# Kernel tuning notes

Measured on AMD Instinct MI355X. Metric: run time of the kernel, lower is better.

## Reference

```python
import jax, jax.numpy as jnp
import numpy as np

N_EMBD = 768
N_HEAD = 12
HEAD_DIM = N_EMBD // N_HEAD
B, T = 2, 2048
EPS = 1e-5


def setup_inputs() -> dict:
    key = jax.random.key(0)
    ks = jax.random.split(key, 16)
    s = 0.02
    return {
        "x": jax.random.normal(ks[0], (B, T, N_EMBD), dtype=jnp.float32),
        "ln1_g": jnp.ones((N_EMBD,), jnp.float32),
        "ln1_b": jnp.zeros((N_EMBD,), jnp.float32),
        "W_attn": jax.random.normal(ks[1], (N_EMBD, 3 * N_EMBD), jnp.float32) * s,
        "b_attn": jnp.zeros((3 * N_EMBD,), jnp.float32),
        "W_cproj": jax.random.normal(ks[2], (N_EMBD, N_EMBD), jnp.float32) * s,
        "b_cproj": jnp.zeros((N_EMBD,), jnp.float32),
        "ln2_g": jnp.ones((N_EMBD,), jnp.float32),
        "ln2_b": jnp.zeros((N_EMBD,), jnp.float32),
        "W_fc": jax.random.normal(ks[3], (N_EMBD, 4 * N_EMBD), jnp.float32) * s,
        "b_fc": jnp.zeros((4 * N_EMBD,), jnp.float32),
        "W_mproj": jax.random.normal(ks[4], (4 * N_EMBD, N_EMBD), jnp.float32) * s,
        "b_mproj": jnp.zeros((N_EMBD,), jnp.float32),
    }


def _layernorm(x, g, b):
    mu = jnp.mean(x, axis=-1, keepdims=True)
    var = jnp.mean(jnp.square(x - mu), axis=-1, keepdims=True)
    return (x - mu) * jax.lax.rsqrt(var + EPS) * g + b


def _attention(h, W_attn, b_attn, W_cproj, b_cproj):
    Bx, Tx, C = h.shape
    qkv = h @ W_attn + b_attn  # [B, T, 3C]
    q, k, v = jnp.split(qkv, 3, axis=-1)
    # [B, H, T, D]
    def split_heads(t):
        return t.reshape(Bx, Tx, N_HEAD, HEAD_DIM).transpose(0, 2, 1, 3)
    q, k, v = split_heads(q), split_heads(k), split_heads(v)
    att = jnp.einsum("bhqd,bhkd->bhqk", q, k) / np.sqrt(HEAD_DIM).astype(np.float32)
    causal = jnp.tril(jnp.ones((Tx, Tx), dtype=bool))
    att = jnp.where(causal, att, jnp.float32(-jnp.inf))
    att = jax.nn.softmax(att, axis=-1)
    y = jnp.einsum("bhqk,bhkd->bhqd", att, v)
    y = y.transpose(0, 2, 1, 3).reshape(Bx, Tx, C)
    return y @ W_cproj + b_cproj


def _mlp(h, W_fc, b_fc, W_mproj, b_mproj):
    return jax.nn.gelu(h @ W_fc + b_fc, approximate=False) @ W_mproj + b_mproj


def reference(x, ln1_g, ln1_b, W_attn, b_attn, W_cproj, b_cproj,
              ln2_g, ln2_b, W_fc, b_fc, W_mproj, b_mproj):
    x = x + _attention(_layernorm(x, ln1_g, ln1_b), W_attn, b_attn, W_cproj, b_cproj)
    x = x + _mlp(_layernorm(x, ln2_g, ln2_b), W_fc, b_fc, W_mproj, b_mproj)
    return x
```

## Files before the change

kernel.cpp:

```cpp
#include <hip/hip_runtime.h>
#include <cstdint>
#include <cstddef>

#define B_ 2
#define T_ 2048
#define C_ 768
#define H_ 12
#define D_ 64

typedef __attribute__((ext_vector_type(8))) short s16x8;
typedef __attribute__((ext_vector_type(4))) float fx4;

static __device__ __forceinline__ unsigned short f2bf(float f) {
  unsigned u = __builtin_bit_cast(unsigned, f);
  unsigned r = u + 0x7fffu + ((u >> 16) & 1u);
  return (unsigned short)(r >> 16);
}
static __device__ __forceinline__ unsigned short f2bf_trunc(float f) {
  return (unsigned short)(__builtin_bit_cast(unsigned, f) >> 16);
}

static __device__ __forceinline__ void glds16(const unsigned short* g, unsigned short* l) {
  __builtin_amdgcn_global_load_lds(
      (const __attribute__((address_space(1))) void*)(g),
      (__attribute__((address_space(3))) void*)(l), 16, 0, 0);
}

__global__ __launch_bounds__(256) void prep(
    const float* __restrict__ Wattn, const float* __restrict__ Wcproj,
    const float* __restrict__ Wfc, const float* __restrict__ Wmproj,
    unsigned short* __restrict__ WattnT, unsigned short* __restrict__ WcprojT,
    unsigned short* __restrict__ WfcT, unsigned short* __restrict__ WmprojT,
    const float* __restrict__ X, const float* __restrict__ g,
    const float* __restrict__ bb, unsigned short* __restrict__ O) {
  __shared__ float tile[32][33];
  __shared__ float ps[8];
  int bid = blockIdx.x, tid = threadIdx.x;
  if (bid < 6912) {
    const float* W; unsigned short* Wt; int R, C, idx;
    if (bid < 1728)      { W = Wattn;  Wt = WattnT;  R = 768;  C = 2304; idx = bid; }
    else if (bid < 2304) { W = Wcproj; Wt = WcprojT; R = 768;  C = 768;  idx = bid - 1728; }
    else if (bid < 4608) { W = Wfc;    Wt = WfcT;    R = 768;  C = 3072; idx = bid - 2304; }
    else                 { W = Wmproj; Wt = WmprojT; R = 3072; C = 768;  idx = bid - 4608; }
    int ct = C >> 5;
    int c0 = (idx % ct) * 32, r0 = (idx / ct) * 32;
    int tx = tid & 31, ty = tid >> 5;
#pragma unroll
    for (int i = 0; i < 4; ++i)
      tile[ty + i * 8][tx] = W[(size_t)(r0 + ty + i * 8) * C + (c0 + tx)];
    __syncthreads();
#pragma unroll
    for (int i = 0; i < 4; ++i)
      Wt[(size_t)(c0 + ty + i * 8) * R + (r0 + tx)] = f2bf(tile[tx][ty + i * 8]);
  } else {
    int row = bid - 6912;
    const float* xr = X + (size_t)row * C_;
    float v0 = xr[tid], v1 = xr[tid + 256], v2 = xr[tid + 512];
    float s = v0 + v1 + v2;
    float s2 = v0 * v0 + v1 * v1 + v2 * v2;
#pragma unroll
    for (int off = 1; off < 64; off <<= 1) {
      s += __shfl_xor(s, off);
      s2 += __shfl_xor(s2, off);
    }
    int wv = tid >> 6;
    if ((tid & 63) == 0) { ps[wv] = s; ps[wv + 4] = s2; }
    __syncthreads();
    s = ps[0] + ps[1] + ps[2] + ps[3];
    s2 = ps[4] + ps[5] + ps[6] + ps[7];
    float mu = s * (1.f / C_);
    float var = s2 * (1.f / C_) - mu * mu;
    float rstd = rsqrtf(var + 1e-5f);
    unsigned short* orow = O + (size_t)row * C_;
    orow[tid]       = f2bf((v0 - mu) * rstd * g[tid]       + bb[tid]);
    orow[tid + 256] = f2bf((v1 - mu) * rstd * g[tid + 256] + bb[tid + 256]);
    orow[tid + 512] = f2bf((v2 - mu) * rstd * g[tid + 512] + bb[tid + 512]);
  }
}

__global__ __launch_bounds__(256) void layernorm_bf16(
    const float* __restrict__ X, const float* __restrict__ g,
    const float* __restrict__ bb, unsigned short* __restrict__ O) {
  int row = blockIdx.x, tid = threadIdx.x;
  const float* xr = X + (size_t)row * C_;
  float v0 = xr[tid], v1 = xr[tid + 256], v2 = xr[tid + 512];
  float s = v0 + v1 + v2;
  float s2 = v0 * v0 + v1 * v1 + v2 * v2;
#pragma unroll
  for (int off = 1; off < 64; off <<= 1) {
    s += __shfl_xor(s, off);
    s2 += __shfl_xor(s2, off);
  }
  __shared__ float ps[8];
  int wv = tid >> 6;
  if ((tid & 63) == 0) { ps[wv] = s; ps[wv + 4] = s2; }
  __syncthreads();
  s = ps[0] + ps[1] + ps[2] + ps[3];
  s2 = ps[4] + ps[5] + ps[6] + ps[7];
  float mu = s * (1.f / C_);
  float var = s2 * (1.f / C_) - mu * mu;
  float rstd = rsqrtf(var + 1e-5f);
  unsigned short* orow = O + (size_t)row * C_;
  orow[tid]       = f2bf((v0 - mu) * rstd * g[tid]       + bb[tid]);
  orow[tid + 256] = f2bf((v1 - mu) * rstd * g[tid + 256] + bb[tid + 256]);
  orow[tid + 512] = f2bf((v2 - mu) * rstd * g[tid + 512] + bb[tid + 512]);
}

template <int BM, int BN, int BK, int MODE>
__global__ __launch_bounds__(256) void gemm_db(
    const unsigned short* __restrict__ A, const unsigned short* __restrict__ Bt,
    const float* __restrict__ bias, const float* __restrict__ resid,
    float* __restrict__ outF, unsigned short* __restrict__ outB,
    unsigned short* __restrict__ qO, unsigned short* __restrict__ kO,
    unsigned short* __restrict__ vtO, int M, int N, int K) {
  constexpr int AT = BM / 32;
  constexpr int BT = BN / 32;
  constexpr int KS = BK / 32;
  constexpr int CA = BM * BK / 2048;
  constexpr int CB = BN * BK / 2048;
  constexpr int ASZ = BM * BK, BSZ = BN * BK;
  constexpr bool SWIZ = (BK == 64);
  __shared__ __align__(16) unsigned short As[2 * ASZ];
  __shared__ __align__(16) unsigned short Bs[2 * BSZ];
  int tid = threadIdx.x;
  int wv = tid >> 6, lane = tid & 63, quad = lane >> 4, l15 = lane & 15;
  int wm = wv >> 1, wn = wv & 1;
  int m0, n0;
  if (MODE == 1) { m0 = blockIdx.x * BM; n0 = blockIdx.y * BN; }
  else           { n0 = blockIdx.x * BN; m0 = blockIdx.y * BM; }
  fx4 acc[AT][BT];
#pragma unroll
  for (int i = 0; i < AT; ++i)
#pragma unroll
    for (int j = 0; j < BT; ++j) acc[i][j] = fx4{0.f, 0.f, 0.f, 0.f};

  int nk = K / BK;
#pragma unroll
  for (int i = 0; i < CA; ++i) {
    int e = (i * 256 + tid) * 8;
    int row = e / BK, col = e & (BK - 1);
    if (SWIZ) col = (((col >> 3) ^ (row & 7)) << 3);
    glds16(&A[(size_t)(m0 + row) * K + col], &As[(i * 256 + (tid & ~63)) * 8]);
  }
#pragma unroll
  for (int i = 0; i < CB; ++i) {
    int e = (i * 256 + tid) * 8;
    int row = e / BK, col = e & (BK - 1);
    if (SWIZ) col = (((col >> 3) ^ (row & 7)) << 3);
    glds16(&Bt[(size_t)(n0 + row) * K + col], &Bs[(i * 256 + (tid & ~63)) * 8]);
  }
  for (int kt = 0; kt < nk; ++kt) {
    int cur = kt & 1;
    __syncthreads();
    if (kt + 1 < nk) {
      int kb = (kt + 1) * BK;
      int nxt = cur ^ 1;
#pragma unroll
      for (int i = 0; i < CA; ++i) {
        int e = (i * 256 + tid) * 8;
        int row = e / BK, col = e & (BK - 1);
        if (SWIZ) col = (((col >> 3) ^ (row & 7)) << 3);
        glds16(&A[(size_t)(m0 + row) * K + kb + col],
               &As[nxt * ASZ + (i * 256 + (tid & ~63)) * 8]);
      }
#pragma unroll
      for (int i = 0; i < CB; ++i) {
        int e = (i * 256 + tid) * 8;
        int row = e / BK, col = e & (BK - 1);
        if (SWIZ) col = (((col >> 3) ^ (row & 7)) << 3);
        glds16(&Bt[(size_t)(n0 + row) * K + kb + col],
               &Bs[nxt * BSZ + (i * 256 + (tid & ~63)) * 8]);
      }
    }
#pragma unroll
    for (int ks = 0; ks < KS; ++ks) {
      s16x8 af[AT], bf[BT];
#pragma unroll
      for (int mt = 0; mt < AT; ++mt) {
        int r = wm * (BM / 2) + mt * 16 + l15;
        int c = ks * 32 + quad * 8;
        if (SWIZ) c = (((c >> 3) ^ (r & 7)) << 3);
        af[mt] = *(const s16x8*)&As[cur * ASZ + r * BK + c];
      }
#pragma unroll
      for (int nt = 0; nt < BT; ++nt) {
        int r = wn * (BN / 2) + nt * 16 + l15;
        int c = ks * 32 + quad * 8;
        if (SWIZ) c = (((c >> 3) ^ (r & 7)) << 3);
        bf[nt] = *(const s16x8*)&Bs[cur * BSZ + r * BK + c];
      }
#pragma unroll
      for (int mt = 0; mt < AT; ++mt)
#pragma unroll
        for (int nt = 0; nt < BT; ++nt)
          acc[mt][nt] = __builtin_amdgcn_mfma_f32_16x16x32_bf16(af[mt], bf[nt], acc[mt][nt], 0, 0, 0);
    }
  }

#pragma unroll
  for (int mt = 0; mt < AT; ++mt)
#pragma unroll
    for (int nt = 0; nt < BT; ++nt) {
      int mb = m0 + wm * (BM / 2) + mt * 16 + quad * 4;
      int n = n0 + wn * (BN / 2) + nt * 16 + l15;
      if (MODE == 0) {
        int which = n / C_;
        int within = n - which * C_;
        int hd = within >> 6, d = within & 63;
        int bbx = mb >> 11, t = mb & 2047;
        size_t bh = (size_t)(bbx * H_ + hd);
        float b = bias[n];
        if (which == 2) {
          unsigned v01 = (unsigned)f2bf(acc[mt][nt][0] + b) |
                         ((unsigned)f2bf(acc[mt][nt][1] + b) << 16);
          unsigned v23 = (unsigned)f2bf(acc[mt][nt][2] + b) |
                         ((unsigned)f2bf(acc[mt][nt][3] + b) << 16);
          *(uint2*)&vtO[(bh * D_ + d) * T_ + t] = uint2{v01, v23};
        } else {
          unsigned short* dst = (which == 0) ? qO : kO;
#pragma unroll
          for (int r = 0; r < 4; ++r)
            dst[(bh * T_ + t + r) * D_ + d] = f2bf(acc[mt][nt][r] + b);
        }
      } else if (MODE == 1) {
#pragma unroll
        for (int r = 0; r < 4; ++r) {
          int m = mb + r;
          float v = acc[mt][nt][r] + bias[n];
          outF[(size_t)m * N + n] = resid[(size_t)m * N + n] + v;
        }
      } else {
#pragma unroll
        for (int r = 0; r < 4; ++r) {
          int m = mb + r;
          float v = acc[mt][nt][r] + bias[n];
          float gl = 0.5f * v * (1.f + erff(v * 0.70710678118654752f));
          outB[(size_t)m * N + n] = f2bf(gl);
        }
      }
    }
}

__global__ __launch_bounds__(256) void attn_fused(
    const unsigned short* __restrict__ Q, const unsigned short* __restrict__ Kg,
    const unsigned short* __restrict__ Vt, unsigned short* __restrict__ Y) {
  __shared__ __align__(16) unsigned short Ks[64 * 72];
  __shared__ __align__(16) unsigned short Vs[64 * 72];
  __shared__ __align__(16) unsigned short Ps[4][16 * 72];
  int tid = threadIdx.x;
  int wv = tid >> 6, lane = tid & 63, quad = lane >> 4, l15 = lane & 15;
  int l = blockIdx.x;
  int w = l >> 8, c = l & 255;
  int i = c & 31;
  int bh = w * 8 + (c >> 5);
  int qt;
  if (w == 0)      qt = i;
  else if (w == 1) qt = (i + 16) & 31;
  else             qt = (i < 16) ? (30 - 2 * i) : (63 - 2 * i);
  int bbx = bh / H_, hh = bh - bbx * H_;
  int q0 = qt * 64;
  size_t base = (size_t)bh * T_ * D_;
  size_t vbase = (size_t)bh * D_ * T_;
  int qrow = q0 + wv * 16 + l15;
  s16x8 qf0 = *(const s16x8*)&Q[base + (size_t)qrow * D_ + quad * 8];
  s16x8 qf1 = *(const s16x8*)&Q[base + (size_t)qrow * D_ + 32 + quad * 8];
  float lsum[4];
  fx4 oacc[4];
#pragma unroll
  for (int t = 0; t < 4; ++t) {
    lsum[t] = 0.f;
    oacc[t] = fx4{0.f, 0.f, 0.f, 0.f};
  }
  int r0s = tid >> 3;
  int c8 = (tid & 7) * 8;
  uint4 ka, kc, va, vc;
  {
    ka = *(const uint4*)&Kg[base + (size_t)r0s * D_ + c8];
    kc = *(const uint4*)&Kg[base + (size_t)(r0s + 32) * D_ + c8];
    va = *(const uint4*)&Vt[vbase + (size_t)r0s * T_ + c8];
    vc = *(const uint4*)&Vt[vbase + (size_t)(r0s + 32) * T_ + c8];
  }
  for (int kb = 0; kb <= qt; ++kb) {
    int k0 = kb * 64;
    __syncthreads();
    *(uint4*)&Ks[r0s * 72 + c8] = ka;
    *(uint4*)&Ks[(r0s + 32) * 72 + c8] = kc;
    *(uint4*)&Vs[r0s * 72 + c8] = va;
    *(uint4*)&Vs[(r0s + 32) * 72 + c8] = vc;
    __syncthreads();
    if (kb < qt) {
      int kn = k0 + 64;
      ka = *(const uint4*)&Kg[base + (size_t)(kn + r0s) * D_ + c8];
      kc = *(const uint4*)&Kg[base + (size_t)(kn + r0s + 32) * D_ + c8];
      va = *(const uint4*)&Vt[vbase + (size_t)r0s * T_ + kn + c8];
      vc = *(const uint4*)&Vt[vbase + (size_t)(r0s + 32) * T_ + kn + c8];
    }
    fx4 sc[4];
#pragma unroll
    for (int nt = 0; nt < 4; ++nt) {
      sc[nt] = fx4{0.f, 0.f, 0.f, 0.f};
      s16x8 kf0 = *(const s16x8*)&Ks[(nt * 16 + l15) * 72 + quad * 8];
      s16x8 kf1 = *(const s16x8*)&Ks[(nt * 16 + l15) * 72 + 32 + quad * 8];
      sc[nt] = __builtin_amdgcn_mfma_f32_16x16x32_bf16(qf0, kf0, sc[nt], 0, 0, 0);
      sc[nt] = __builtin_amdgcn_mfma_f32_16x16x32_bf16(qf1, kf1, sc[nt], 0, 0, 0);
    }
    bool diag = (kb == qt);
    unsigned short* pw = &Ps[wv][0];
#pragma unroll
    for (int nt = 0; nt < 4; ++nt)
#pragma unroll
      for (int r = 0; r < 4; ++r) {
        float p;
        if (diag && (k0 + nt * 16 + l15) > (q0 + wv * 16 + quad * 4 + r)) {
          p = 0.f;
        } else {
          p = __expf(sc[nt][r] * 0.125f);
        }
        lsum[r] += p;
        pw[(quad * 4 + r) * 72 + nt * 16 + l15] = f2bf_trunc(p);
      }
    s16x8 pa0 = *(const s16x8*)&pw[l15 * 72 + quad * 8];
    s16x8 pa1 = *(const s16x8*)&pw[l15 * 72 + 32 + quad * 8];
#pragma unroll
    for (int nt = 0; nt < 4; ++nt) {
      s16x8 vf0 = *(const s16x8*)&Vs[(nt * 16 + l15) * 72 + quad * 8];
      s16x8 vf1 = *(const s16x8*)&Vs[(nt * 16 + l15) * 72 + 32 + quad * 8];
      oacc[nt] = __builtin_amdgcn_mfma_f32_16x16x32_bf16(pa0, vf0, oacc[nt], 0, 0, 0);
      oacc[nt] = __builtin_amdgcn_mfma_f32_16x16x32_bf16(pa1, vf1, oacc[nt], 0, 0, 0);
    }
  }
#pragma unroll
  for (int r = 0; r < 4; ++r) {
#pragma unroll
    for (int off = 1; off < 16; off <<= 1) lsum[r] += __shfl_xor(lsum[r], off);
  }
#pragma unroll
  for (int nt = 0; nt < 4; ++nt)
#pragma unroll
    for (int r = 0; r < 4; ++r) {
      float o = oacc[nt][r] / lsum[r];
      int token = bbx * T_ + q0 + wv * 16 + quad * 4 + r;
      Y[(size_t)token * C_ + hh * D_ + nt * 16 + l15] = f2bf(o);
    }
}

extern "C" void kernel_launch(void* const* d_in, const int* in_sizes, int n_in,
                              void* d_out, int out_size, void* d_ws, size_t ws_size,
                              hipStream_t stream) {
  const float* x      = (const float*)d_in[0];
  const float* ln1g   = (const float*)d_in[1];
  const float* ln1b   = (const float*)d_in[2];
  const float* Wattn  = (const float*)d_in[3];
  const float* battn  = (const float*)d_in[4];
  const float* Wcproj = (const float*)d_in[5];
  const float* bcproj = (const float*)d_in[6];
  const float* ln2g   = (const float*)d_in[7];
  const float* ln2b   = (const float*)d_in[8];
  const float* Wfc    = (const float*)d_in[9];
  const float* bfc    = (const float*)d_in[10];
  const float* Wmproj = (const float*)d_in[11];
  const float* bmproj = (const float*)d_in[12];
  float* out = (float*)d_out;
  char* ws = (char*)d_ws;

  unsigned short* WattnT  = (unsigned short*)(ws + 0);
  unsigned short* WcprojT = (unsigned short*)(ws + 3538944);
  unsigned short* WfcT    = (unsigned short*)(ws + 4718592);
  unsigned short* WmprojT = (unsigned short*)(ws + 9437184);
  unsigned short* hbuf    = (unsigned short*)(ws + 14155776);
  unsigned short* Qb      = (unsigned short*)(ws + 20447232);
  unsigned short* Kb      = (unsigned short*)(ws + 26738688);
  unsigned short* Vtb     = (unsigned short*)(ws + 33030144);
  unsigned short* Yb      = (unsigned short*)(ws + 39321600);
  float*          x1      = (float*)(ws + 45613056);
  unsigned short* Ab      = (unsigned short*)(ws + 58195968);

  prep<<<11008, 256, 0, stream>>>(Wattn, Wcproj, Wfc, Wmproj,
                                  WattnT, WcprojT, WfcT, WmprojT,
                                  x, ln1g, ln1b, hbuf);

  gemm_db<128, 96, 64, 0><<<dim3(24, 32), 256, 0, stream>>>(
      hbuf, WattnT, battn, nullptr, nullptr, nullptr, Qb, Kb, Vtb, 4096, 2304, 768);

  attn_fused<<<768, 256, 0, stream>>>(Qb, Kb, Vtb, Yb);

  gemm_db<128, 96, 64, 1><<<dim3(32, 8), 256, 0, stream>>>(
      Yb, WcprojT, bcproj, x, x1, nullptr, nullptr, nullptr, nullptr, 4096, 768, 768);

  layernorm_bf16<<<4096, 256, 0, stream>>>(x1, ln2g, ln2b, hbuf);

  gemm_db<128, 128, 32, 2><<<dim3(24, 32), 256, 0, stream>>>(
      hbuf, WfcT, bfc, nullptr, nullptr, Ab, nullptr, nullptr, nullptr, 4096, 3072, 768);

  gemm_db<128, 96, 64, 1><<<dim3(32, 8), 256, 0, stream>>>(
      Ab, WmprojT, bmproj, x1, out, nullptr, nullptr, nullptr, nullptr, 4096, 768, 3072);
}
```

Baseline: 271.2 us.

## Split-K the MLP down-projection and retune GEMM tile shapes

Adds a split-K mode for the 3072-deep MLP projection. Two K halves each write fp32 partials, and a new reduce kernel adds them together with the residual and bias. This raises the block count from 256 to 768 on a chip with many CUs, which should improve occupancy. The c_proj GEMM moves to 128x64 tiles for more blocks, and the QKV GEMM drops to BK=32. The cost is an extra kernel launch plus partial-sum traffic through workspace that reuses the Q buffer region.

```diff
diff --git a/kernel.cpp b/kernel.cpp
--- a/kernel.cpp
+++ b/kernel.cpp
@@ -106,18 +106,34 @@
   orow[tid + 512] = f2bf((v2 - mu) * rstd * g[tid + 512] + bb[tid + 512]);
 }
 
+__global__ __launch_bounds__(256) void reduce_out(
+    const float* __restrict__ x1, const float* __restrict__ P,
+    const float* __restrict__ bias, float* __restrict__ out) {
+  int idx = blockIdx.x * 256 + threadIdx.x;
+  float4 a = ((const float4*)x1)[idx];
+  float4 p = ((const float4*)P)[idx];
+  float4 q = ((const float4*)(P + (size_t)4096 * 768))[idx];
+  float4 b = ((const float4*)bias)[idx % 192];
+  float4 o;
+  o.x = a.x + p.x + q.x + b.x;
+  o.y = a.y + p.y + q.y + b.y;
+  o.z = a.z + p.z + q.z + b.z;
+  o.w = a.w + p.w + q.w + b.w;
+  ((float4*)out)[idx] = o;
+}
+
 template <int BM, int BN, int BK, int MODE>
 __global__ __launch_bounds__(256) void gemm_db(
     const unsigned short* __restrict__ A, const unsigned short* __restrict__ Bt,
     const float* __restrict__ bias, const float* __restrict__ resid,
     float* __restrict__ outF, unsigned short* __restrict__ outB,
     unsigned short* __restrict__ qO, unsigned short* __restrict__ kO,
-    unsigned short* __restrict__ vtO, int M, int N, int K) {
+    unsigned short* __restrict__ vtO, int M, int N, int K, int KC) {
   constexpr int AT = BM / 32;
   constexpr int BT = BN / 32;
   constexpr int KS = BK / 32;
-  constexpr int CA = BM * BK / 2048;
-  constexpr int CB = BN * BK / 2048;
+  constexpr int ACH = BM * BK / 8;
+  constexpr int BCH = BN * BK / 8;
   constexpr int ASZ = BM * BK, BSZ = BN * BK;
   constexpr bool SWIZ = (BK == 64);
   __shared__ __align__(16) unsigned short As[2 * ASZ];
@@ -126,29 +142,33 @@
   int wv = tid >> 6, lane = tid & 63, quad = lane >> 4, l15 = lane & 15;
   int wm = wv >> 1, wn = wv & 1;
   int m0, n0;
-  if (MODE == 1) { m0 = blockIdx.x * BM; n0 = blockIdx.y * BN; }
-  else           { n0 = blockIdx.x * BN; m0 = blockIdx.y * BM; }
+  if (MODE == 1 || MODE == 3) { m0 = blockIdx.x * BM; n0 = blockIdx.y * BN; }
+  else                        { n0 = blockIdx.x * BN; m0 = blockIdx.y * BM; }
+  const unsigned short* Ak = A + (size_t)blockIdx.z * KC;
+  const unsigned short* Bk = Bt + (size_t)blockIdx.z * KC;
   fx4 acc[AT][BT];
 #pragma unroll
   for (int i = 0; i < AT; ++i)
 #pragma unroll
     for (int j = 0; j < BT; ++j) acc[i][j] = fx4{0.f, 0.f, 0.f, 0.f};
 
-  int nk = K / BK;
-#pragma unroll
-  for (int i = 0; i < CA; ++i) {
-    int e = (i * 256 + tid) * 8;
-    int row = e / BK, col = e & (BK - 1);
-    if (SWIZ) col = (((col >> 3) ^ (row & 7)) << 3);
-    glds16(&A[(size_t)(m0 + row) * K + col], &As[(i * 256 + (tid & ~63)) * 8]);
-  }
-#pragma unroll
-  for (int i = 0; i < CB; ++i) {
-    int e = (i * 256 + tid) * 8;
-    int row = e / BK, col = e & (BK - 1);
-    if (SWIZ) col = (((col >> 3) ^ (row & 7)) << 3);
-    glds16(&Bt[(size_t)(n0 + row) * K + col], &Bs[(i * 256 + (tid & ~63)) * 8]);
-  }
+  int nk = KC / BK;
+#pragma unroll
+  for (int i0 = 0; i0 < ACH; i0 += 256)
+    if (ACH - i0 >= 256 || tid < ACH - i0) {
+      int e = (i0 + tid) * 8;
+      int row = e / BK, col = e & (BK - 1);
+      if (SWIZ) col = (((col >> 3) ^ (row & 7)) << 3);
+      glds16(&Ak[(size_t)(m0 + row) * K + col], &As[(i0 + (tid & ~63)) * 8]);
+    }
+#pragma unroll
+  for (int i0 = 0; i0 < BCH; i0 += 256)
+    if (BCH - i0 >= 256 || tid < BCH - i0) {
+      int e = (i0 + tid) * 8;
+      int row = e / BK, col = e & (BK - 1);
+      if (SWIZ) col = (((col >> 3) ^ (row & 7)) << 3);
+      glds16(&Bk[(size_t)(n0 + row) * K + col], &Bs[(i0 + (tid & ~63)) * 8]);
+    }
   for (int kt = 0; kt < nk; ++kt) {
     int cur = kt & 1;
     __syncthreads();
@@ -156,21 +176,23 @@
       int kb = (kt + 1) * BK;
       int nxt = cur ^ 1;
 #pragma unroll
-      for (int i = 0; i < CA; ++i) {
-        int e = (i * 256 + tid) * 8;
-        int row = e / BK, col = e & (BK - 1);
-        if (SWIZ) col = (((col >> 3) ^ (row & 7)) << 3);
-        glds16(&A[(size_t)(m0 + row) * K + kb + col],
-               &As[nxt * ASZ + (i * 256 + (tid & ~63)) * 8]);
-      }
-#pragma unroll
-      for (int i = 0; i < CB; ++i) {
-        int e = (i * 256 + tid) * 8;
-        int row = e / BK, col = e & (BK - 1);
-        if (SWIZ) col = (((col >> 3) ^ (row & 7)) << 3);
-        glds16(&Bt[(size_t)(n0 + row) * K + kb + col],
-               &Bs[nxt * BSZ + (i * 256 + (tid & ~63)) * 8]);
-      }
+      for (int i0 = 0; i0 < ACH; i0 += 256)
+        if (ACH - i0 >= 256 || tid < ACH - i0) {
+          int e = (i0 + tid) * 8;
+          int row = e / BK, col = e & (BK - 1);
+          if (SWIZ) col = (((col >> 3) ^ (row & 7)) << 3);
+          glds16(&Ak[(size_t)(m0 + row) * K + kb + col],
+                 &As[nxt * ASZ + (i0 + (tid & ~63)) * 8]);
+        }
+#pragma unroll
+      for (int i0 = 0; i0 < BCH; i0 += 256)
+        if (BCH - i0 >= 256 || tid < BCH - i0) {
+          int e = (i0 + tid) * 8;
+          int row = e / BK, col = e & (BK - 1);
+          if (SWIZ) col = (((col >> 3) ^ (row & 7)) << 3);
+          glds16(&Bk[(size_t)(n0 + row) * K + kb + col],
+                 &Bs[nxt * BSZ + (i0 + (tid & ~63)) * 8]);
+        }
     }
 #pragma unroll
     for (int ks = 0; ks < KS; ++ks) {
@@ -229,6 +251,11 @@
           float v = acc[mt][nt][r] + bias[n];
           outF[(size_t)m * N + n] = resid[(size_t)m * N + n] + v;
         }
+      } else if (MODE == 3) {
+        float* P = outF + (size_t)blockIdx.z * M * N;
+#pragma unroll
+        for (int r = 0; r < 4; ++r)
+          P[(size_t)(mb + r) * N + n] = acc[mt][nt][r];
       } else {
 #pragma unroll
         for (int r = 0; r < 4; ++r) {
@@ -374,24 +401,31 @@
   unsigned short* Yb      = (unsigned short*)(ws + 39321600);
   float*          x1      = (float*)(ws + 45613056);
   unsigned short* Ab      = (unsigned short*)(ws + 58195968);
+  float*          Pbuf    = (float*)(ws + 20447232);
 
   prep<<<11008, 256, 0, stream>>>(Wattn, Wcproj, Wfc, Wmproj,
                                   WattnT, WcprojT, WfcT, WmprojT,
                                   x, ln1g, ln1b, hbuf);
 
-  gemm_db<128, 96, 64, 0><<<dim3(24, 32), 256, 0, stream>>>(
-      hbuf, WattnT, battn, nullptr, nullptr, nullptr, Qb, Kb, Vtb, 4096, 2304, 768);
+  gemm_db<128, 96, 32, 0><<<dim3(24, 32), 256, 0, stream>>>(
+      hbuf, WattnT, battn, nullptr, nullptr, nullptr, Qb, Kb, Vtb,
+      4096, 2304, 768, 768);
 
   attn_fused<<<768, 256, 0, stream>>>(Qb, Kb, Vtb, Yb);
 
-  gemm_db<128, 96, 64, 1><<<dim3(32, 8), 256, 0, stream>>>(
-      Yb, WcprojT, bcproj, x, x1, nullptr, nullptr, nullptr, nullptr, 4096, 768, 768);
+  gemm_db<128, 64, 64, 1><<<dim3(32, 12), 256, 0, stream>>>(
+      Yb, WcprojT, bcproj, x, x1, nullptr, nullptr, nullptr, nullptr,
+      4096, 768, 768, 768);
 
   layernorm_bf16<<<4096, 256, 0, stream>>>(x1, ln2g, ln2b, hbuf);
 
   gemm_db<128, 128, 32, 2><<<dim3(24, 32), 256, 0, stream>>>(
-      hbuf, WfcT, bfc, nullptr, nullptr, Ab, nullptr, nullptr, nullptr, 4096, 3072, 768);
-
-  gemm_db<128, 96, 64, 1><<<dim3(32, 8), 256, 0, stream>>>(
-      Ab, WmprojT, bmproj, x1, out, nullptr, nullptr, nullptr, nullptr, 4096, 768, 3072);
-}
+      hbuf, WfcT, bfc, nullptr, nullptr, Ab, nullptr, nullptr, nullptr,
+      4096, 3072, 768, 768);
+
+  gemm_db<128, 64, 64, 3><<<dim3(32, 12, 2), 256, 0, stream>>>(
+      Ab, WmprojT, bmproj, nullptr, Pbuf, nullptr, nullptr, nullptr, nullptr,
+      4096, 768, 3072, 1536);
+
+  reduce_out<<<3072, 256, 0, stream>>>(x1, Pbuf, bmproj, out);
+}
```

New measurement: 259.3 us. 1.05x faster.
